# Performance work log

Hardware: AMD Instinct MI355X
Metric: run time of the kernel (lower is better)

## Reference

```python
import jax, jax.numpy as jnp
import numpy as np

T, B, X, Y = 24, 16, 64, 64
S, M, C = 16, 8, 8
F = S + M + C   # GRU input_size = 32
H = 32          # hidden_size


def setup_inputs() -> dict:
    key = jax.random.key(0)
    ks = jax.random.split(key, 8)
    inv = 1.0 / np.sqrt(H)
    return {
        "spatial": jax.random.normal(ks[0], (T, B, X, Y, S), dtype=jnp.float32),
        "meteorology": jax.random.normal(ks[1], (T, B, X, Y, M), dtype=jnp.float32),
        "context": jax.random.normal(ks[2], (T, B, X, Y, C), dtype=jnp.float32),
        # GRU parameters (torch layout: [3H, F] and [3H, H], gate order r,z,n)
        "W_ih": jax.random.uniform(ks[3], (3 * H, F), jnp.float32, -inv, inv),
        "W_hh": jax.random.uniform(ks[4], (3 * H, H), jnp.float32, -inv, inv),
        "b_ih": jax.random.uniform(ks[5], (3 * H,), jnp.float32, -inv, inv),
        "b_hh": jax.random.uniform(ks[6], (3 * H,), jnp.float32, -inv, inv),
        # output projection (hidden -> spatial_size)
        "W": jax.random.normal(ks[7], (H, S), dtype=jnp.float32),
    }


def reference(spatial, meteorology, context, W_ih, W_hh, b_ih, b_hh, W):
    # cat features: (T, B, X, Y, F); merge all pixels + batch into one GRU batch
    x = jnp.concatenate((spatial, meteorology, context), axis=4)
    N = B * X * Y
    x = x.reshape(T, N, F)

    # precompute input projections for all timesteps: (T, N, 3H)
    gx_all = jnp.einsum('tnf,gf->tng', x, W_ih) + b_ih

    def step(h, gx):
        gh = h @ W_hh.T + b_hh                      # (N, 3H)
        r = jax.nn.sigmoid(gx[:, :H] + gh[:, :H])
        z = jax.nn.sigmoid(gx[:, H:2 * H] + gh[:, H:2 * H])
        n = jnp.tanh(gx[:, 2 * H:] + r * gh[:, 2 * H:])
        h = (1.0 - z) * n + z * h
        return h, None

    h0 = jnp.zeros((N, H), dtype=x.dtype)
    h_final, _ = jax.lax.scan(step, h0, gx_all)     # (N, H)

    out = h_final @ W                               # (N, S)
    return out.reshape(B, X, Y, S)
```

## Files before the change

kernel.cpp:

```cpp
#include <hip/hip_runtime.h>
#include <hip/hip_bf16.h>


#define TSTEPS 24
#define NPIX 65536
#define PADW 40

typedef __attribute__((ext_vector_type(8))) short bf16x8;
typedef __attribute__((ext_vector_type(4))) float f32x4;
typedef __attribute__((ext_vector_type(4))) unsigned int u32x4;

#define MFMA16(a, b, c) __builtin_amdgcn_mfma_f32_16x16x32_bf16((a), (b), (c), 0, 0, 0)

__device__ __forceinline__ unsigned short f2bf(float f) {
  unsigned u = __builtin_bit_cast(unsigned, f);
  u += 0x7fffu + ((u >> 16) & 1u);
  return (unsigned short)(u >> 16);
}

__device__ __forceinline__ unsigned pk2(float a, float b) {
  __hip_bfloat162 h = __float22bfloat162_rn(float2{a, b});
  unsigned u;
  __builtin_memcpy(&u, &h, sizeof(u));
  return u;
}

__device__ __forceinline__ bf16x8 pack8(f32x4 a, f32x4 b) {
  u32x4 r = { pk2(a[0], a[1]), pk2(a[2], a[3]), pk2(b[0], b[1]), pk2(b[2], b[3]) };
  return __builtin_bit_cast(bf16x8, r);
}

__device__ __forceinline__ float sigmoid_(float x) {
  return __builtin_amdgcn_rcpf(1.f + __expf(-x));
}
__device__ __forceinline__ float tanh_(float x) {
  return 1.f - 2.f * __builtin_amdgcn_rcpf(__expf(2.f * x) + 1.f);
}

__device__ __forceinline__ bf16x8 relayout_h(const f32x4 h0, const f32x4 h1, int lane) {
  unsigned p00 = pk2(h0[0], h0[1]), p01 = pk2(h0[2], h0[3]);
  unsigned p10 = pk2(h1[0], h1[1]), p11 = pk2(h1[2], h1[3]);
  const int lo = (lane & 15) | ((lane & 16) << 1);
  const int hi = lo + 16;
  unsigned a0 = (unsigned)__shfl((int)p00, lo, 64);
  unsigned a1 = (unsigned)__shfl((int)p01, lo, 64);
  unsigned a2 = (unsigned)__shfl((int)p00, hi, 64);
  unsigned a3 = (unsigned)__shfl((int)p01, hi, 64);
  unsigned b0 = (unsigned)__shfl((int)p10, lo, 64);
  unsigned b1 = (unsigned)__shfl((int)p11, lo, 64);
  unsigned b2 = (unsigned)__shfl((int)p10, hi, 64);
  unsigned b3 = (unsigned)__shfl((int)p11, hi, 64);
  const bool t1 = (lane & 32) != 0;
  u32x4 d = { t1 ? b0 : a0, t1 ? b1 : a1, t1 ? b2 : a2, t1 ? b3 : a3 };
  return __builtin_bit_cast(bf16x8, d);
}

__global__ __launch_bounds__(256, 2)
void gru_fused(const float* __restrict__ spatial, const float* __restrict__ met,
               const float* __restrict__ ctx,
               const float* __restrict__ W_ih, const float* __restrict__ W_hh,
               const float* __restrict__ b_ih, const float* __restrict__ b_hh,
               const float* __restrict__ Wout, float* __restrict__ out) {
  __shared__ __align__(16) unsigned short sW[192 * PADW];
  __shared__ __align__(16) float sCB[64];
  __shared__ __align__(16) float sBIN[32];
  __shared__ __align__(16) float sBHN[32];

  const int tid = threadIdx.x;
  for (int i = tid; i < 96 * 32; i += 256) {
    int r = i >> 5, c = i & 31;
    sW[r * PADW + c] = f2bf(W_ih[i]);
    sW[(96 + r) * PADW + c] = f2bf(W_hh[i]);
  }
  if (tid < 64) sCB[tid] = b_ih[tid] + b_hh[tid];
  else if (tid < 96) sBIN[tid - 64] = b_ih[tid];
  else if (tid < 128) sBHN[tid - 96] = b_hh[tid - 32];
  __syncthreads();

  const int lane = tid & 63;
  const int col = lane & 15;
  const int q = lane >> 4;
  const int wave = blockIdx.x * 4 + (tid >> 6);
  const long p0 = (long)wave * 32 + col;
  const long p1 = p0 + 16;

  f32x4 cS[4];
#pragma unroll
  for (int i = 0; i < 4; ++i) cS[i] = *(const f32x4*)&sCB[i * 16 + q * 4];
  const f32x4 cG4 = *(const f32x4*)&sBIN[q * 4];
  const f32x4 cG5 = *(const f32x4*)&sBIN[16 + q * 4];
  const f32x4 cH4 = *(const f32x4*)&sBHN[q * 4];
  const f32x4 cH5 = *(const f32x4*)&sBHN[16 + q * 4];

  const float *xp0, *xp1;
  long xstride;
  if (q < 2) {
    xp0 = spatial + p0 * 16 + q * 8; xp1 = spatial + p1 * 16 + q * 8;
    xstride = (long)NPIX * 16;
  } else if (q == 2) {
    xp0 = met + p0 * 8; xp1 = met + p1 * 8; xstride = (long)NPIX * 8;
  } else {
    xp0 = ctx + p0 * 8; xp1 = ctx + p1 * 8; xstride = (long)NPIX * 8;
  }

  bf16x8 bx0 = pack8(*(const f32x4*)xp0, *(const f32x4*)(xp0 + 4));
  bf16x8 bx1 = pack8(*(const f32x4*)xp1, *(const f32x4*)(xp1 + 4));
  xp0 += xstride; xp1 += xstride;

  f32x4 h0a = {0.f, 0.f, 0.f, 0.f}, h0b = {0.f, 0.f, 0.f, 0.f};
  f32x4 h1a = {0.f, 0.f, 0.f, 0.f}, h1b = {0.f, 0.f, 0.f, 0.f};
  const f32x4 zero = {0.f, 0.f, 0.f, 0.f};

  const int wb = col * PADW + q * 8;

#pragma unroll 1
  for (int t = 0; t < TSTEPS; ++t) {
    f32x4 xn0a, xn0b, xn1a, xn1b;
    if (t < TSTEPS - 1) {
      xn0a = *(const f32x4*)xp0; xn0b = *(const f32x4*)(xp0 + 4);
      xn1a = *(const f32x4*)xp1; xn1b = *(const f32x4*)(xp1 + 4);
      xp0 += xstride; xp1 += xstride;
    }

    bf16x8 bh0 = relayout_h(h0a, h0b, lane);
    bf16x8 bh1 = relayout_h(h1a, h1b, lane);

    bf16x8 a0 = *(const bf16x8*)&sW[wb];
    bf16x8 a1 = *(const bf16x8*)&sW[wb + 16 * PADW];
    bf16x8 a2 = *(const bf16x8*)&sW[wb + 32 * PADW];
    bf16x8 a3 = *(const bf16x8*)&sW[wb + 48 * PADW];
    bf16x8 a4 = *(const bf16x8*)&sW[wb + 64 * PADW];
    bf16x8 a5 = *(const bf16x8*)&sW[wb + 80 * PADW];
    bf16x8 w0 = *(const bf16x8*)&sW[wb + 96 * PADW];
    bf16x8 w1 = *(const bf16x8*)&sW[wb + 112 * PADW];
    bf16x8 w2 = *(const bf16x8*)&sW[wb + 128 * PADW];
    bf16x8 w3 = *(const bf16x8*)&sW[wb + 144 * PADW];
    bf16x8 w4 = *(const bf16x8*)&sW[wb + 160 * PADW];
    bf16x8 w5 = *(const bf16x8*)&sW[wb + 176 * PADW];

    f32x4 G0[6], H0[6], G1[6], H1[6];
    G0[0] = MFMA16(a0, bx0, cS[0]);  G1[0] = MFMA16(a0, bx1, cS[0]);
    G0[1] = MFMA16(a1, bx0, cS[1]);  G1[1] = MFMA16(a1, bx1, cS[1]);
    G0[2] = MFMA16(a2, bx0, cS[2]);  G1[2] = MFMA16(a2, bx1, cS[2]);
    G0[3] = MFMA16(a3, bx0, cS[3]);  G1[3] = MFMA16(a3, bx1, cS[3]);
    G0[4] = MFMA16(a4, bx0, cG4);    G1[4] = MFMA16(a4, bx1, cG4);
    G0[5] = MFMA16(a5, bx0, cG5);    G1[5] = MFMA16(a5, bx1, cG5);
    H0[0] = MFMA16(w0, bh0, zero);   H1[0] = MFMA16(w0, bh1, zero);
    H0[1] = MFMA16(w1, bh0, zero);   H1[1] = MFMA16(w1, bh1, zero);
    H0[2] = MFMA16(w2, bh0, zero);   H1[2] = MFMA16(w2, bh1, zero);
    H0[3] = MFMA16(w3, bh0, zero);   H1[3] = MFMA16(w3, bh1, zero);
    H0[4] = MFMA16(w4, bh0, cH4);    H1[4] = MFMA16(w4, bh1, cH4);
    H0[5] = MFMA16(w5, bh0, cH5);    H1[5] = MFMA16(w5, bh1, cH5);

#pragma unroll
    for (int r = 0; r < 4; ++r) {
      float r00 = sigmoid_(G0[0][r] + H0[0][r]);
      float r01 = sigmoid_(G0[1][r] + H0[1][r]);
      float z00 = sigmoid_(G0[2][r] + H0[2][r]);
      float z01 = sigmoid_(G0[3][r] + H0[3][r]);
      float n00 = tanh_(G0[4][r] + r00 * H0[4][r]);
      float n01 = tanh_(G0[5][r] + r01 * H0[5][r]);
      h0a[r] = n00 + z00 * (h0a[r] - n00);
      h0b[r] = n01 + z01 * (h0b[r] - n01);

      float r10 = sigmoid_(G1[0][r] + H1[0][r]);
      float r11 = sigmoid_(G1[1][r] + H1[1][r]);
      float z10 = sigmoid_(G1[2][r] + H1[2][r]);
      float z11 = sigmoid_(G1[3][r] + H1[3][r]);
      float n10 = tanh_(G1[4][r] + r10 * H1[4][r]);
      float n11 = tanh_(G1[5][r] + r11 * H1[5][r]);
      h1a[r] = n10 + z10 * (h1a[r] - n10);
      h1b[r] = n11 + z11 * (h1b[r] - n11);
    }

    if (t < TSTEPS - 1) {
      bx0 = pack8(xn0a, xn0b);
      bx1 = pack8(xn1a, xn1b);
    }
  }

  bf16x8 bhf0 = relayout_h(h0a, h0b, lane);
  bf16x8 bhf1 = relayout_h(h1a, h1b, lane);
  float w[8];
#pragma unroll
  for (int j = 0; j < 8; ++j) w[j] = Wout[(q * 8 + j) * 16 + col];
  u32x4 awp = { pk2(w[0], w[1]), pk2(w[2], w[3]), pk2(w[4], w[5]), pk2(w[6], w[7]) };
  bf16x8 aw = __builtin_bit_cast(bf16x8, awp);
  f32x4 o0 = MFMA16(aw, bhf0, zero);
  f32x4 o1 = MFMA16(aw, bhf1, zero);
  *(f32x4*)&out[p0 * 16 + q * 4] = o0;
  *(f32x4*)&out[p1 * 16 + q * 4] = o1;
}

extern "C" void kernel_launch(void* const* d_in, const int* in_sizes, int n_in,
                              void* d_out, int out_size, void* d_ws, size_t ws_size,
                              hipStream_t stream) {
  const float* spatial = (const float*)d_in[0];
  const float* met     = (const float*)d_in[1];
  const float* ctx     = (const float*)d_in[2];
  const float* W_ih    = (const float*)d_in[3];
  const float* W_hh    = (const float*)d_in[4];
  const float* b_ih    = (const float*)d_in[5];
  const float* b_hh    = (const float*)d_in[6];
  const float* Wout    = (const float*)d_in[7];
  float* out = (float*)d_out;

  gru_fused<<<dim3(NPIX / 32 / 4), dim3(256), 0, stream>>>(
      spatial, met, ctx, W_ih, W_hh, b_ih, b_hh, Wout, out);
}
```

Baseline: 233.1 us.

## Fold activation scales into weights, chain MFMAs, one pixel tile per wave

Weights and biases are pre-scaled by -log2(e) for the r/z gates and 2·log2(e) for the n gate, so sigmoid and tanh reduce to exp2 plus rcp with no extra multiply. The r/z gate MFMAs now accumulate the input projection directly into the hidden projection. The 12 weight fragments are loaded from LDS once, outside the time loop. Each wave handles 16 pixels instead of 32 and the grid doubles, with launch bounds raised to 3 blocks per SIMD to trade per-wave ILP for more occupancy.

```diff
diff --git a/kernel.cpp b/kernel.cpp
--- a/kernel.cpp
+++ b/kernel.cpp
@@ -11,6 +11,9 @@
 typedef __attribute__((ext_vector_type(4))) unsigned int u32x4;
 
 #define MFMA16(a, b, c) __builtin_amdgcn_mfma_f32_16x16x32_bf16((a), (b), (c), 0, 0, 0)
+
+#define SCL_RZ (-1.4426950408889634f)
+#define SCL_N  ( 2.8853900817779268f)
 
 __device__ __forceinline__ unsigned short f2bf(float f) {
   unsigned u = __builtin_bit_cast(unsigned, f);
@@ -30,11 +33,11 @@
   return __builtin_bit_cast(bf16x8, r);
 }
 
-__device__ __forceinline__ float sigmoid_(float x) {
-  return __builtin_amdgcn_rcpf(1.f + __expf(-x));
+__device__ __forceinline__ float sig2(float t) {
+  return __builtin_amdgcn_rcpf(1.f + __builtin_amdgcn_exp2f(t));
 }
-__device__ __forceinline__ float tanh_(float x) {
-  return 1.f - 2.f * __builtin_amdgcn_rcpf(__expf(2.f * x) + 1.f);
+__device__ __forceinline__ float tanh2(float t) {
+  return 1.f - 2.f * __builtin_amdgcn_rcpf(1.f + __builtin_amdgcn_exp2f(t));
 }
 
 __device__ __forceinline__ bf16x8 relayout_h(const f32x4 h0, const f32x4 h1, int lane) {
@@ -55,7 +58,7 @@
   return __builtin_bit_cast(bf16x8, d);
 }
 
-__global__ __launch_bounds__(256, 2)
+__global__ __launch_bounds__(256, 3)
 void gru_fused(const float* __restrict__ spatial, const float* __restrict__ met,
                const float* __restrict__ ctx,
                const float* __restrict__ W_ih, const float* __restrict__ W_hh,
@@ -69,20 +72,20 @@
   const int tid = threadIdx.x;
   for (int i = tid; i < 96 * 32; i += 256) {
     int r = i >> 5, c = i & 31;
-    sW[r * PADW + c] = f2bf(W_ih[i]);
-    sW[(96 + r) * PADW + c] = f2bf(W_hh[i]);
+    float s = (r < 64) ? SCL_RZ : SCL_N;
+    sW[r * PADW + c] = f2bf(W_ih[i] * s);
+    sW[(96 + r) * PADW + c] = f2bf(W_hh[i] * s);
   }
-  if (tid < 64) sCB[tid] = b_ih[tid] + b_hh[tid];
-  else if (tid < 96) sBIN[tid - 64] = b_ih[tid];
-  else if (tid < 128) sBHN[tid - 96] = b_hh[tid - 32];
+  if (tid < 64) sCB[tid] = (b_ih[tid] + b_hh[tid]) * SCL_RZ;
+  else if (tid < 96) sBIN[tid - 64] = b_ih[tid] * SCL_N;
+  else if (tid < 128) sBHN[tid - 96] = b_hh[tid - 32] * SCL_N;
   __syncthreads();
 
   const int lane = tid & 63;
   const int col = lane & 15;
   const int q = lane >> 4;
   const int wave = blockIdx.x * 4 + (tid >> 6);
-  const long p0 = (long)wave * 32 + col;
-  const long p1 = p0 + 16;
+  const long p0 = (long)wave * 16 + col;
 
   f32x4 cS[4];
 #pragma unroll
@@ -92,104 +95,84 @@
   const f32x4 cH4 = *(const f32x4*)&sBHN[q * 4];
   const f32x4 cH5 = *(const f32x4*)&sBHN[16 + q * 4];
 
-  const float *xp0, *xp1;
+  const int wb = col * PADW + q * 8;
+  const bf16x8 a0 = *(const bf16x8*)&sW[wb];
+  const bf16x8 a1 = *(const bf16x8*)&sW[wb + 16 * PADW];
+  const bf16x8 a2 = *(const bf16x8*)&sW[wb + 32 * PADW];
+  const bf16x8 a3 = *(const bf16x8*)&sW[wb + 48 * PADW];
+  const bf16x8 a4 = *(const bf16x8*)&sW[wb + 64 * PADW];
+  const bf16x8 a5 = *(const bf16x8*)&sW[wb + 80 * PADW];
+  const bf16x8 w0 = *(const bf16x8*)&sW[wb + 96 * PADW];
+  const bf16x8 w1 = *(const bf16x8*)&sW[wb + 112 * PADW];
+  const bf16x8 w2 = *(const bf16x8*)&sW[wb + 128 * PADW];
+  const bf16x8 w3 = *(const bf16x8*)&sW[wb + 144 * PADW];
+  const bf16x8 w4 = *(const bf16x8*)&sW[wb + 160 * PADW];
+  const bf16x8 w5 = *(const bf16x8*)&sW[wb + 176 * PADW];
+
+  const float* xp0;
   long xstride;
   if (q < 2) {
-    xp0 = spatial + p0 * 16 + q * 8; xp1 = spatial + p1 * 16 + q * 8;
+    xp0 = spatial + p0 * 16 + q * 8;
     xstride = (long)NPIX * 16;
   } else if (q == 2) {
-    xp0 = met + p0 * 8; xp1 = met + p1 * 8; xstride = (long)NPIX * 8;
+    xp0 = met + p0 * 8; xstride = (long)NPIX * 8;
   } else {
-    xp0 = ctx + p0 * 8; xp1 = ctx + p1 * 8; xstride = (long)NPIX * 8;
+    xp0 = ctx + p0 * 8; xstride = (long)NPIX * 8;
   }
 
-  bf16x8 bx0 = pack8(*(const f32x4*)xp0, *(const f32x4*)(xp0 + 4));
-  bf16x8 bx1 = pack8(*(const f32x4*)xp1, *(const f32x4*)(xp1 + 4));
-  xp0 += xstride; xp1 += xstride;
+  bf16x8 bx = pack8(*(const f32x4*)xp0, *(const f32x4*)(xp0 + 4));
+  xp0 += xstride;
 
   f32x4 h0a = {0.f, 0.f, 0.f, 0.f}, h0b = {0.f, 0.f, 0.f, 0.f};
-  f32x4 h1a = {0.f, 0.f, 0.f, 0.f}, h1b = {0.f, 0.f, 0.f, 0.f};
   const f32x4 zero = {0.f, 0.f, 0.f, 0.f};
-
-  const int wb = col * PADW + q * 8;
 
 #pragma unroll 1
   for (int t = 0; t < TSTEPS; ++t) {
-    f32x4 xn0a, xn0b, xn1a, xn1b;
+    f32x4 xna, xnb;
     if (t < TSTEPS - 1) {
-      xn0a = *(const f32x4*)xp0; xn0b = *(const f32x4*)(xp0 + 4);
-      xn1a = *(const f32x4*)xp1; xn1b = *(const f32x4*)(xp1 + 4);
-      xp0 += xstride; xp1 += xstride;
+      xna = *(const f32x4*)xp0; xnb = *(const f32x4*)(xp0 + 4);
+      xp0 += xstride;
     }
 
-    bf16x8 bh0 = relayout_h(h0a, h0b, lane);
-    bf16x8 bh1 = relayout_h(h1a, h1b, lane);
+    f32x4 g0 = MFMA16(a0, bx, cS[0]);
+    f32x4 g1 = MFMA16(a1, bx, cS[1]);
+    f32x4 g2 = MFMA16(a2, bx, cS[2]);
+    f32x4 g3 = MFMA16(a3, bx, cS[3]);
+    f32x4 g4 = MFMA16(a4, bx, cG4);
+    f32x4 g5 = MFMA16(a5, bx, cG5);
 
-    bf16x8 a0 = *(const bf16x8*)&sW[wb];
-    bf16x8 a1 = *(const bf16x8*)&sW[wb + 16 * PADW];
-    bf16x8 a2 = *(const bf16x8*)&sW[wb + 32 * PADW];
-    bf16x8 a3 = *(const bf16x8*)&sW[wb + 48 * PADW];
-    bf16x8 a4 = *(const bf16x8*)&sW[wb + 64 * PADW];
-    bf16x8 a5 = *(const bf16x8*)&sW[wb + 80 * PADW];
-    bf16x8 w0 = *(const bf16x8*)&sW[wb + 96 * PADW];
-    bf16x8 w1 = *(const bf16x8*)&sW[wb + 112 * PADW];
-    bf16x8 w2 = *(const bf16x8*)&sW[wb + 128 * PADW];
-    bf16x8 w3 = *(const bf16x8*)&sW[wb + 144 * PADW];
-    bf16x8 w4 = *(const bf16x8*)&sW[wb + 160 * PADW];
-    bf16x8 w5 = *(const bf16x8*)&sW[wb + 176 * PADW];
+    bf16x8 bh = relayout_h(h0a, h0b, lane);
 
-    f32x4 G0[6], H0[6], G1[6], H1[6];
-    G0[0] = MFMA16(a0, bx0, cS[0]);  G1[0] = MFMA16(a0, bx1, cS[0]);
-    G0[1] = MFMA16(a1, bx0, cS[1]);  G1[1] = MFMA16(a1, bx1, cS[1]);
-    G0[2] = MFMA16(a2, bx0, cS[2]);  G1[2] = MFMA16(a2, bx1, cS[2]);
-    G0[3] = MFMA16(a3, bx0, cS[3]);  G1[3] = MFMA16(a3, bx1, cS[3]);
-    G0[4] = MFMA16(a4, bx0, cG4);    G1[4] = MFMA16(a4, bx1, cG4);
-    G0[5] = MFMA16(a5, bx0, cG5);    G1[5] = MFMA16(a5, bx1, cG5);
-    H0[0] = MFMA16(w0, bh0, zero);   H1[0] = MFMA16(w0, bh1, zero);
-    H0[1] = MFMA16(w1, bh0, zero);   H1[1] = MFMA16(w1, bh1, zero);
-    H0[2] = MFMA16(w2, bh0, zero);   H1[2] = MFMA16(w2, bh1, zero);
-    H0[3] = MFMA16(w3, bh0, zero);   H1[3] = MFMA16(w3, bh1, zero);
-    H0[4] = MFMA16(w4, bh0, cH4);    H1[4] = MFMA16(w4, bh1, cH4);
-    H0[5] = MFMA16(w5, bh0, cH5);    H1[5] = MFMA16(w5, bh1, cH5);
+    f32x4 r0 = MFMA16(w0, bh, g0);
+    f32x4 r1 = MFMA16(w1, bh, g1);
+    f32x4 z0 = MFMA16(w2, bh, g2);
+    f32x4 z1 = MFMA16(w3, bh, g3);
+    f32x4 h4 = MFMA16(w4, bh, cH4);
+    f32x4 h5 = MFMA16(w5, bh, cH5);
 
 #pragma unroll
     for (int r = 0; r < 4; ++r) {
-      float r00 = sigmoid_(G0[0][r] + H0[0][r]);
-      float r01 = sigmoid_(G0[1][r] + H0[1][r]);
-      float z00 = sigmoid_(G0[2][r] + H0[2][r]);
-      float z01 = sigmoid_(G0[3][r] + H0[3][r]);
-      float n00 = tanh_(G0[4][r] + r00 * H0[4][r]);
-      float n01 = tanh_(G0[5][r] + r01 * H0[5][r]);
-      h0a[r] = n00 + z00 * (h0a[r] - n00);
-      h0b[r] = n01 + z01 * (h0b[r] - n01);
-
-      float r10 = sigmoid_(G1[0][r] + H1[0][r]);
-      float r11 = sigmoid_(G1[1][r] + H1[1][r]);
-      float z10 = sigmoid_(G1[2][r] + H1[2][r]);
-      float z11 = sigmoid_(G1[3][r] + H1[3][r]);
-      float n10 = tanh_(G1[4][r] + r10 * H1[4][r]);
-      float n11 = tanh_(G1[5][r] + r11 * H1[5][r]);
-      h1a[r] = n10 + z10 * (h1a[r] - n10);
-      h1b[r] = n11 + z11 * (h1b[r] - n11);
+      float ra = sig2(r0[r]);
+      float rb = sig2(r1[r]);
+      float za = sig2(z0[r]);
+      float zb = sig2(z1[r]);
+      float na = tanh2(__builtin_fmaf(ra, h4[r], g4[r]));
+      float nb = tanh2(__builtin_fmaf(rb, h5[r], g5[r]));
+      h0a[r] = na + za * (h0a[r] - na);
+      h0b[r] = nb + zb * (h0b[r] - nb);
     }
 
-    if (t < TSTEPS - 1) {
-      bx0 = pack8(xn0a, xn0b);
-      bx1 = pack8(xn1a, xn1b);
-    }
+    if (t < TSTEPS - 1) bx = pack8(xna, xnb);
   }
 
-  bf16x8 bhf0 = relayout_h(h0a, h0b, lane);
-  bf16x8 bhf1 = relayout_h(h1a, h1b, lane);
+  bf16x8 bhf = relayout_h(h0a, h0b, lane);
   float w[8];
 #pragma unroll
   for (int j = 0; j < 8; ++j) w[j] = Wout[(q * 8 + j) * 16 + col];
   u32x4 awp = { pk2(w[0], w[1]), pk2(w[2], w[3]), pk2(w[4], w[5]), pk2(w[6], w[7]) };
   bf16x8 aw = __builtin_bit_cast(bf16x8, awp);
-  f32x4 o0 = MFMA16(aw, bhf0, zero);
-  f32x4 o1 = MFMA16(aw, bhf1, zero);
+  f32x4 o0 = MFMA16(aw, bhf, zero);
   *(f32x4*)&out[p0 * 16 + q * 4] = o0;
-  *(f32x4*)&out[p1 * 16 + q * 4] = o1;
 }
 
 extern "C" void kernel_launch(void* const* d_in, const int* in_sizes, int n_in,
@@ -205,6 +188,6 @@
   const float* Wout    = (const float*)d_in[7];
   float* out = (float*)d_out;
 
-  gru_fused<<<dim3(NPIX / 32 / 4), dim3(256), 0, stream>>>(
+  gru_fused<<<dim3(NPIX / 16 / 4), dim3(256), 0, stream>>>(
       spatial, met, ctx, W_ih, W_hh, b_ih, b_hh, Wout, out);
 }
```

After: 240.8 us. 1.03x slower.
